# Kernel optimization log

Measured on AMD Instinct MI355X. Metric: run time of the kernel, lower is better.

Reference implementation:

```python
import jax, jax.numpy as jnp
import numpy as np

F = 2048          # frame length = len(window_function) = n_fft
HOP = F // 2      # step_length (overlap=2, perfect reconstruction)
B = 8             # signals / channels
T = 1 << 20       # samples per signal (multiple of HOP)


def setup_inputs() -> dict:
    key = jax.random.key(0)
    x = jax.random.normal(key, (B, T), dtype=jnp.float32)
    # cosine (sine) window, the standard MDCT deringing window
    n = jnp.arange(F, dtype=jnp.float32)
    window = jnp.sin(jnp.pi * (n + 0.5) / F).astype(jnp.float32)
    return {"x": x, "window": window}


def reference(x, window):
    # Batched, fused version of the serial per-frame twiddle-FFT-twiddle MDCT.
    F_ = window.shape[0]
    hop = F_ // 2
    N = F_ // 2                      # output bins per frame (odd-stacked)
    # center=True: pad F/2 zeros on both sides so first/last frames are centered
    xp = jnp.pad(x, ((0, 0), (hop, hop)))
    n_frames = (xp.shape[1] - F_) // hop + 1
    starts = jnp.arange(n_frames) * hop                       # [nf]
    frames = xp[:, starts[:, None] + jnp.arange(F_)]          # [B, nf, F]
    # pre-twiddle: exp(-i*pi*n/(2N)), n = 0..2N-1
    pre = jnp.exp(-1j * jnp.pi * jnp.arange(F_) / F_).astype(jnp.complex64)
    # post-twiddle: exp(-i*pi*n0*(k+0.5)/N), n0 = (N+1)/2
    n0 = (N + 1) / 2.0
    post = jnp.exp(-1j * jnp.pi * n0 * (jnp.arange(N) + 0.5) / N).astype(jnp.complex64)
    # window + pre-twiddle, one batched FFT over all frames, truncate to N bins
    Xc = jnp.fft.fft((frames * window).astype(jnp.complex64) * pre, axis=-1)[..., :N]
    # real part * post-twiddle phase, scale sqrt(1/N)*sqrt(2)
    out = jnp.real(Xc * post) * np.float32(np.sqrt(2.0 / N))
    return out.astype(jnp.float32)          # [B, n_frames, N]
```

## Files before the change

### kernel.cpp

```cpp
#include <hip/hip_runtime.h>
#include <cmath>

#define BATCH   8
#define TLEN    1048576
#define NFRM    1025
#define MROWS   (BATCH * NFRM)

#define SWZ(i) ((i) ^ (((i) >> 4) & 15))

#define CK_1024 0.99999529380957619f
#define SK_1024 0.00306795676296598f
#define C8_1 0.92387953251128674f
#define S8_1 0.38268343236508978f
#define C8_2 0.70710678118654752f
#define S8_2 0.70710678118654752f
#define C8_3 0.38268343236508978f
#define S8_3 0.92387953251128674f

__global__ __launch_bounds__(128)
void mdct_fft_kernel(const float* __restrict__ x,
                     const float* __restrict__ w,
                     float* __restrict__ out)
{
    __shared__ float2 zz[2][2][512];
    const int wid  = threadIdx.x >> 6;
    const int lane = threadIdx.x & 63;
    float2* const za = zz[wid][0];
    float2* const zb = zz[wid][1];
    float*  const uf = (float*)zz[wid][1];

    const int r = blockIdx.x * 2 + wid;
    const int b = r / NFRM;
    const int t = r - b * NFRM;

    const float* xb = x + b * TLEN + (t - 1) * 1024;

#pragma unroll
    for (int sl = 0; sl < 2; ++sl) {
        const int tt = lane + sl * 64;
        {
            const int p  = tt * 4;
            float4 res = {0.0f, 0.0f, 0.0f, 0.0f};
            if (t != NFRM - 1) {
                const int rb = 1532 - p;
                const int fb = 1536 + p;
                float4 xr = *(const float4*)(xb + rb);
                float4 wr = *(const float4*)(w  + rb);
                float4 xf = *(const float4*)(xb + fb);
                float4 wf = *(const float4*)(w  + fb);
                res.x = -(wr.w * xr.w + wf.x * xf.x);
                res.y = -(wr.z * xr.z + wf.y * xf.y);
                res.z = -(wr.y * xr.y + wf.z * xf.z);
                res.w = -(wr.x * xr.x + wf.w * xf.w);
            }
            *(float4*)&uf[p] = res;
        }
        {
            const int p  = 512 + tt * 4;
            float4 res = {0.0f, 0.0f, 0.0f, 0.0f};
            if (t != 0) {
                const int rb = 1532 - p;
                const int fb = p - 512;
                float4 xr = *(const float4*)(xb + rb);
                float4 wr = *(const float4*)(w  + rb);
                float4 xf = *(const float4*)(xb + fb);
                float4 wf = *(const float4*)(w  + fb);
                res.x = wf.x * xf.x - wr.w * xr.w;
                res.y = wf.y * xf.y - wr.z * xr.z;
                res.z = wf.z * xf.z - wr.y * xr.y;
                res.w = wf.w * xf.w - wr.x * xr.x;
            }
            *(float4*)&uf[p] = res;
        }
    }
    __builtin_amdgcn_wave_barrier();

    float cbv[2], sbv[2];
    float c1v[2], s1v[2];

#pragma unroll
    for (int sl = 0; sl < 2; ++sl) {
        const int tt = lane + sl * 64;
        const float ab = (float)(4 * tt + 1) * (1.0f / 4096.0f);
        const float cb = cospif(ab), sb = sinpif(ab);
        cbv[sl] = cb; sbv[sl] = sb;

        float px[4], py[4];
#pragma unroll
        for (int h = 0; h < 4; ++h) {
            const int n = tt + h * 128;
            float re = uf[2 * n];
            float im = uf[1023 - 2 * n];
            float c, s;
            if      (h == 0) { c = cb;                      s = sb; }
            else if (h == 1) { c = cb * C8_1 - sb * S8_1;   s = sb * C8_1 + cb * S8_1; }
            else if (h == 2) { c = cb * C8_2 - sb * S8_2;   s = sb * C8_2 + cb * S8_2; }
            else             { c = cb * C8_3 - sb * S8_3;   s = sb * C8_3 + cb * S8_3; }
            px[h] = re * c + im * s;
            py[h] = im * c - re * s;
        }
        const float c2b = cb * cb - sb * sb, s2b = 2.0f * cb * sb;
        const float c4  = c2b * c2b - s2b * s2b, s4 = 2.0f * c2b * s2b;
        const float c1  = c4 * CK_1024 + s4 * SK_1024;
        const float s1  = s4 * CK_1024 - c4 * SK_1024;
        c1v[sl] = c1; s1v[sl] = s1;
        const float c2 = c1 * c1 - s1 * s1, s2 = 2.0f * c1 * s1;
        const float c3 = c1 * c2 - s1 * s2, s3 = s1 * c2 + c1 * s2;

        float sax = px[0] + px[2], say = py[0] + py[2];
        float sbx = px[1] + px[3], sby = py[1] + py[3];
        float dax = px[0] - px[2], day = py[0] - py[2];
        float dbx = px[1] - px[3], dby = py[1] - py[3];
        const int o = 4 * tt;
        za[SWZ(o)] = make_float2(sax + sbx, say + sby);
        float e1x = dax + dby, e1y = day - dbx;
        za[SWZ(o + 1)] = make_float2(e1x * c1 + e1y * s1, e1y * c1 - e1x * s1);
        float e2x = sax - sbx, e2y = say - sby;
        za[SWZ(o + 2)] = make_float2(e2x * c2 + e2y * s2, e2y * c2 - e2x * s2);
        float e3x = dax - dby, e3y = day + dbx;
        za[SWZ(o + 3)] = make_float2(e3x * c3 + e3y * s3, e3y * c3 - e3x * s3);
    }
    __builtin_amdgcn_wave_barrier();

    float2* X = za;
    float2* Y = zb;
#pragma unroll
    for (int j = 1; j < 4; ++j) {
        const int ls = 2 * j;
        const int s  = 1 << ls;
#pragma unroll
        for (int sl = 0; sl < 2; ++sl) {
            const int tt = lane + sl * 64;
            const int p  = tt >> ls;
            float2 P0 = X[SWZ(tt)];
            float2 P1 = X[SWZ(tt + 128)];
            float2 P2 = X[SWZ(tt + 256)];
            float2 P3 = X[SWZ(tt + 384)];
            const int q = (tt >> (2 * j - 2)) & 3;
            float cd, sd;
            if (j == 1) {
                cd = q == 0 ? 1.0f : q == 1 ? 0.99992470183914450f
                   : q == 2 ? 0.99969881869620422f : 0.99932238458834954f;
                sd = q == 0 ? 0.0f : q == 1 ? 0.01227153828571993f
                   : q == 2 ? 0.02454122852291229f : 0.03680722294135883f;
            } else if (j == 2) {
                cd = q == 0 ? 1.0f : q == 1 ? 0.99879545620517241f
                   : q == 2 ? 0.99518472667219693f : 0.98917650996478101f;
                sd = q == 0 ? 0.0f : q == 1 ? 0.04906767432741802f
                   : q == 2 ? 0.09801714032956060f : 0.14673047445536175f;
            } else {
                cd = q == 0 ? 1.0f : q == 1 ? 0.98078528040323044f
                   : q == 2 ? 0.92387953251128674f : 0.83146961230254524f;
                sd = q == 0 ? 0.0f : q == 1 ? 0.19509032201612825f
                   : q == 2 ? 0.38268343236508978f : 0.55557023301960222f;
            }
            const float c1 = c1v[sl] * cd + s1v[sl] * sd;
            const float s1 = s1v[sl] * cd - c1v[sl] * sd;
            c1v[sl] = c1; s1v[sl] = s1;
            const float c2 = c1 * c1 - s1 * s1, s2 = 2.0f * c1 * s1;
            const float c3 = c1 * c2 - s1 * s2, s3 = s1 * c2 + c1 * s2;

            float sax = P0.x + P2.x, say = P0.y + P2.y;
            float sbx = P1.x + P3.x, sby = P1.y + P3.y;
            float dax = P0.x - P2.x, day = P0.y - P2.y;
            float dbx = P1.x - P3.x, dby = P1.y - P3.y;
            const int o = tt + 3 * s * p;
            Y[SWZ(o)] = make_float2(sax + sbx, say + sby);
            float e1x = dax + dby, e1y = day - dbx;
            Y[SWZ(o + s)] = make_float2(e1x * c1 + e1y * s1, e1y * c1 - e1x * s1);
            float e2x = sax - sbx, e2y = say - sby;
            Y[SWZ(o + 2 * s)] = make_float2(e2x * c2 + e2y * s2, e2y * c2 - e2x * s2);
            float e3x = dax - dby, e3y = day + dbx;
            Y[SWZ(o + 3 * s)] = make_float2(e3x * c3 + e3y * s3, e3y * c3 - e3x * s3);
        }
        float2* tmp = X; X = Y; Y = tmp;
        __builtin_amdgcn_wave_barrier();
    }

    float2 Av[4], Bv[4];
#pragma unroll
    for (int sl = 0; sl < 2; ++sl) {
        const int tt = lane + sl * 64;
#pragma unroll
        for (int hh = 0; hh < 2; ++hh) {
            const int k0 = tt + hh * 128;
            Av[sl * 2 + hh] = X[SWZ(k0)];
            Bv[sl * 2 + hh] = X[SWZ(k0 + 256)];
        }
    }
    __builtin_amdgcn_wave_barrier();
#pragma unroll
    for (int sl = 0; sl < 2; ++sl) {
        const int tt = lane + sl * 64;
        const float cb = cbv[sl], sb = sbv[sl];
#pragma unroll
        for (int hh = 0; hh < 2; ++hh) {
            const int k0 = tt + hh * 128;
            const float2 A  = Av[sl * 2 + hh];
            const float2 Bq = Bv[sl * 2 + hh];
            float zr[2] = {A.x + Bq.x, A.x - Bq.x};
            float zi[2] = {A.y + Bq.y, A.y - Bq.y};
#pragma unroll
            for (int h = 0; h < 2; ++h) {
                const int k = k0 + h * 256;
                const int idx = hh + 2 * h;
                float c, s;
                if      (idx == 0) { c = cb;                      s = sb; }
                else if (idx == 1) { c = cb * C8_1 - sb * S8_1;   s = sb * C8_1 + cb * S8_1; }
                else if (idx == 2) { c = cb * C8_2 - sb * S8_2;   s = sb * C8_2 + cb * S8_2; }
                else               { c = cb * C8_3 - sb * S8_3;   s = sb * C8_3 + cb * S8_3; }
                float re = zr[h] * c + zi[h] * s;
                float im = zi[h] * c - zr[h] * s;
                uf[2 * k]        =  re * 0.04419417382415922f;
                uf[1023 - 2 * k] = -im * 0.04419417382415922f;
            }
        }
    }
    __builtin_amdgcn_wave_barrier();

#pragma unroll
    for (int sl = 0; sl < 2; ++sl) {
        const int tt = lane + sl * 64;
        *(float4*)&out[r * 1024 + tt * 4]       = *(const float4*)&uf[tt * 4];
        *(float4*)&out[r * 1024 + 512 + tt * 4] = *(const float4*)&uf[512 + tt * 4];
    }
}

extern "C" void kernel_launch(void* const* d_in, const int* in_sizes, int n_in,
                              void* d_out, int out_size, void* d_ws, size_t ws_size,
                              hipStream_t stream) {
    const float* x = (const float*)d_in[0];
    const float* w = (const float*)d_in[1];
    float* out = (float*)d_out;
    (void)d_ws; (void)ws_size;

    static_assert(MROWS % 2 == 0, "two frames per block");
    mdct_fft_kernel<<<MROWS / 2, 128, 0, stream>>>(x, w, out);
}
```

Measured before the change: 91.61 us.

## Halve LDS per wave with in-place FFT stages and write output directly

Shared memory per wave drops from two 512-entry complex buffers to one. Each radix-4 stage now loads its inputs into registers, waits at a wave barrier, then writes back in place. The final post-twiddle stores scattered scalar values straight to global memory instead of staging them in LDS for float4 stores, and launch bounds now request 6 blocks per SIMD. The aim is higher occupancy and fewer LDS round trips, at the cost of uncoalesced strided global stores and more register pressure.

```diff
diff --git a/kernel.cpp b/kernel.cpp
--- a/kernel.cpp
+++ b/kernel.cpp
@@ -17,17 +17,18 @@
 #define C8_3 0.38268343236508978f
 #define S8_3 0.92387953251128674f
 
-__global__ __launch_bounds__(128)
+#define OUT_SCALE 0.04419417382415922f
+
+__global__ __launch_bounds__(128, 6)
 void mdct_fft_kernel(const float* __restrict__ x,
                      const float* __restrict__ w,
                      float* __restrict__ out)
 {
-    __shared__ float2 zz[2][2][512];
+    __shared__ float2 zz[2][512];
     const int wid  = threadIdx.x >> 6;
     const int lane = threadIdx.x & 63;
-    float2* const za = zz[wid][0];
-    float2* const zb = zz[wid][1];
-    float*  const uf = (float*)zz[wid][1];
+    float2* const za = zz[wid];
+    float*  const uf = (float*)zz[wid];
 
     const int r = blockIdx.x * 2 + wid;
     const int b = r / NFRM;
@@ -78,6 +79,18 @@
     float cbv[2], sbv[2];
     float c1v[2], s1v[2];
 
+    float ure[2][4], uim[2][4];
+#pragma unroll
+    for (int sl = 0; sl < 2; ++sl) {
+        const int tt = lane + sl * 64;
+#pragma unroll
+        for (int h = 0; h < 4; ++h) {
+            const int n = tt + h * 128;
+            ure[sl][h] = uf[2 * n];
+            uim[sl][h] = uf[1023 - 2 * n];
+        }
+    }
+    __builtin_amdgcn_wave_barrier();
 #pragma unroll
     for (int sl = 0; sl < 2; ++sl) {
         const int tt = lane + sl * 64;
@@ -88,16 +101,13 @@
         float px[4], py[4];
 #pragma unroll
         for (int h = 0; h < 4; ++h) {
-            const int n = tt + h * 128;
-            float re = uf[2 * n];
-            float im = uf[1023 - 2 * n];
             float c, s;
             if      (h == 0) { c = cb;                      s = sb; }
             else if (h == 1) { c = cb * C8_1 - sb * S8_1;   s = sb * C8_1 + cb * S8_1; }
             else if (h == 2) { c = cb * C8_2 - sb * S8_2;   s = sb * C8_2 + cb * S8_2; }
             else             { c = cb * C8_3 - sb * S8_3;   s = sb * C8_3 + cb * S8_3; }
-            px[h] = re * c + im * s;
-            py[h] = im * c - re * s;
+            px[h] = ure[sl][h] * c + uim[sl][h] * s;
+            py[h] = uim[sl][h] * c - ure[sl][h] * s;
         }
         const float c2b = cb * cb - sb * sb, s2b = 2.0f * cb * sb;
         const float c4  = c2b * c2b - s2b * s2b, s4 = 2.0f * c2b * s2b;
@@ -122,20 +132,23 @@
     }
     __builtin_amdgcn_wave_barrier();
 
-    float2* X = za;
-    float2* Y = zb;
 #pragma unroll
     for (int j = 1; j < 4; ++j) {
         const int ls = 2 * j;
         const int s  = 1 << ls;
+        float2 P[2][4];
+#pragma unroll
+        for (int sl = 0; sl < 2; ++sl) {
+            const int tt = lane + sl * 64;
+#pragma unroll
+            for (int i = 0; i < 4; ++i)
+                P[sl][i] = za[SWZ(tt + i * 128)];
+        }
+        __builtin_amdgcn_wave_barrier();
 #pragma unroll
         for (int sl = 0; sl < 2; ++sl) {
             const int tt = lane + sl * 64;
             const int p  = tt >> ls;
-            float2 P0 = X[SWZ(tt)];
-            float2 P1 = X[SWZ(tt + 128)];
-            float2 P2 = X[SWZ(tt + 256)];
-            float2 P3 = X[SWZ(tt + 384)];
             const int q = (tt >> (2 * j - 2)) & 3;
             float cd, sd;
             if (j == 1) {
@@ -160,44 +173,32 @@
             const float c2 = c1 * c1 - s1 * s1, s2 = 2.0f * c1 * s1;
             const float c3 = c1 * c2 - s1 * s2, s3 = s1 * c2 + c1 * s2;
 
-            float sax = P0.x + P2.x, say = P0.y + P2.y;
-            float sbx = P1.x + P3.x, sby = P1.y + P3.y;
-            float dax = P0.x - P2.x, day = P0.y - P2.y;
-            float dbx = P1.x - P3.x, dby = P1.y - P3.y;
+            float sax = P[sl][0].x + P[sl][2].x, say = P[sl][0].y + P[sl][2].y;
+            float sbx = P[sl][1].x + P[sl][3].x, sby = P[sl][1].y + P[sl][3].y;
+            float dax = P[sl][0].x - P[sl][2].x, day = P[sl][0].y - P[sl][2].y;
+            float dbx = P[sl][1].x - P[sl][3].x, dby = P[sl][1].y - P[sl][3].y;
             const int o = tt + 3 * s * p;
-            Y[SWZ(o)] = make_float2(sax + sbx, say + sby);
+            za[SWZ(o)] = make_float2(sax + sbx, say + sby);
             float e1x = dax + dby, e1y = day - dbx;
-            Y[SWZ(o + s)] = make_float2(e1x * c1 + e1y * s1, e1y * c1 - e1x * s1);
+            za[SWZ(o + s)] = make_float2(e1x * c1 + e1y * s1, e1y * c1 - e1x * s1);
             float e2x = sax - sbx, e2y = say - sby;
-            Y[SWZ(o + 2 * s)] = make_float2(e2x * c2 + e2y * s2, e2y * c2 - e2x * s2);
+            za[SWZ(o + 2 * s)] = make_float2(e2x * c2 + e2y * s2, e2y * c2 - e2x * s2);
             float e3x = dax - dby, e3y = day + dbx;
-            Y[SWZ(o + 3 * s)] = make_float2(e3x * c3 + e3y * s3, e3y * c3 - e3x * s3);
-        }
-        float2* tmp = X; X = Y; Y = tmp;
+            za[SWZ(o + 3 * s)] = make_float2(e3x * c3 + e3y * s3, e3y * c3 - e3x * s3);
+        }
         __builtin_amdgcn_wave_barrier();
     }
 
-    float2 Av[4], Bv[4];
-#pragma unroll
-    for (int sl = 0; sl < 2; ++sl) {
-        const int tt = lane + sl * 64;
+    float* const ob = out + r * 1024;
+#pragma unroll
+    for (int sl = 0; sl < 2; ++sl) {
+        const int tt = lane + sl * 64;
+        const float cb = cbv[sl], sb = sbv[sl];
 #pragma unroll
         for (int hh = 0; hh < 2; ++hh) {
             const int k0 = tt + hh * 128;
-            Av[sl * 2 + hh] = X[SWZ(k0)];
-            Bv[sl * 2 + hh] = X[SWZ(k0 + 256)];
-        }
-    }
-    __builtin_amdgcn_wave_barrier();
-#pragma unroll
-    for (int sl = 0; sl < 2; ++sl) {
-        const int tt = lane + sl * 64;
-        const float cb = cbv[sl], sb = sbv[sl];
-#pragma unroll
-        for (int hh = 0; hh < 2; ++hh) {
-            const int k0 = tt + hh * 128;
-            const float2 A  = Av[sl * 2 + hh];
-            const float2 Bq = Bv[sl * 2 + hh];
+            const float2 A  = za[SWZ(k0)];
+            const float2 Bq = za[SWZ(k0 + 256)];
             float zr[2] = {A.x + Bq.x, A.x - Bq.x};
             float zi[2] = {A.y + Bq.y, A.y - Bq.y};
 #pragma unroll
@@ -211,18 +212,10 @@
                 else               { c = cb * C8_3 - sb * S8_3;   s = sb * C8_3 + cb * S8_3; }
                 float re = zr[h] * c + zi[h] * s;
                 float im = zi[h] * c - zr[h] * s;
-                uf[2 * k]        =  re * 0.04419417382415922f;
-                uf[1023 - 2 * k] = -im * 0.04419417382415922f;
-            }
-        }
-    }
-    __builtin_amdgcn_wave_barrier();
-
-#pragma unroll
-    for (int sl = 0; sl < 2; ++sl) {
-        const int tt = lane + sl * 64;
-        *(float4*)&out[r * 1024 + tt * 4]       = *(const float4*)&uf[tt * 4];
-        *(float4*)&out[r * 1024 + 512 + tt * 4] = *(const float4*)&uf[512 + tt * 4];
+                ob[2 * k]        =  re * OUT_SCALE;
+                ob[1023 - 2 * k] = -im * OUT_SCALE;
+            }
+        }
     }
 }
 
```

Measured after the change: 91.13 us. About the same (-0.5%).
